# Kernel tuning notes

Hardware: AMD Instinct MI355X
Metric: run time of the kernel (lower is better)

## Reference

```python
import jax, jax.numpy as jnp
import numpy as np

B, S, H, NH = 2, 2048, 1024, 16
HD = H // NH  # 64


def setup_inputs() -> dict:
    key = jax.random.key(0)
    ks = jax.random.split(key, 9)
    s = 1.0 / np.sqrt(H)
    d = {"x": jax.random.normal(ks[0], (B, S, H), jnp.float32)}
    for i, n in enumerate(["Wq", "Wk", "Wv", "Wo"]):
        d[n] = jax.random.normal(ks[1 + i], (H, H), jnp.float32) * s
    for i, n in enumerate(["bq", "bk", "bv", "bo"]):
        d[n] = jax.random.normal(ks[5 + i], (H,), jnp.float32) * s
    return d


def _heads(x, W, b):
    # torch nn.Linear: y = x @ W.T + b, then split heads -> (B, NH, S, HD)
    y = x @ W.T + b
    return y.reshape(B, S, NH, HD).transpose(0, 2, 1, 3)


def _tetra_channels(t):
    # tetrapoint vector [a, 1-a, a*(1-a), clamp(1-(a+(1-a)),0,1)] for a scalar slice t
    a = jax.nn.sigmoid(t)
    na = 1.0 - a
    neither = jnp.clip(1.0 - (a + na), 0.0, 1.0)
    return jnp.stack([a, na, a * na, neither], axis=-1)  # (..., 4)


def reference(x, Wq, bq, Wk, bk, Wv, bv, Wo, bo):
    Q = _heads(x, Wq, bq)  # (B, NH, S, HD)
    K = _heads(x, Wk, bk)
    V = _heads(x, Wv, bv)
    # Original indexes Q_tetrapoints[:, :, :, 0] on [B,NH,S,HD,4]: selects head-dim
    # slot 0 (resp. 2) and keeps the 4 tetrapoint channels -> (B, NH, S, 4).
    Qa = _tetra_channels(Q[..., 0])
    Ka = _tetra_channels(K[..., 0])
    Qb = _tetra_channels(Q[..., 2])
    Kb = _tetra_channels(K[..., 2])
    scores = (jnp.einsum('bhsc,bhtc->bhst', Qa, Ka) / np.sqrt(HD)
              + 0.1 * jnp.einsum('bhsc,bhtc->bhst', Qb, Kb))  # (B, NH, S, S)
    w = jax.nn.softmax(scores, axis=-1)
    out = jnp.einsum('bhst,bhtd->bhsd', w, V)  # (B, NH, S, HD)
    out = out.transpose(0, 2, 1, 3).reshape(B, S, H)
    return out @ Wo.T + bo
```

## Files before the change

kernel.cpp:

```cpp
#include <hip/hip_runtime.h>
#include <hip/hip_bf16.h>

#define SS 2048
#define HH 1024
#define NHH 16
#define HDD 64

using f32x4  = __attribute__((ext_vector_type(4))) float;
using bf16x8 = __attribute__((ext_vector_type(8))) short;

#if __has_builtin(__builtin_amdgcn_exp2f)
#define EXP2F __builtin_amdgcn_exp2f
#else
#define EXP2F exp2f
#endif

__device__ __forceinline__ unsigned short f2bf(float f) {
    unsigned u = __builtin_bit_cast(unsigned, f);
    unsigned r = u + 0x7FFFu + ((u >> 16) & 1u);
    return (unsigned short)(r >> 16);
}

__device__ __forceinline__ unsigned bfround(float f) {
    unsigned u = __builtin_bit_cast(unsigned, f);
    return u + 0x7FFFu + ((u >> 16) & 1u);
}
__device__ __forceinline__ unsigned pack2bf(float a, float b) {
    return __builtin_amdgcn_perm(bfround(b), bfround(a), 0x07060302u);
}
__device__ __forceinline__ unsigned pack2bf_trunc(float a, float b) {
    return __builtin_amdgcn_perm(__builtin_bit_cast(unsigned, b),
                                 __builtin_bit_cast(unsigned, a), 0x07060302u);
}

__device__ __forceinline__ void tetra(float t, float* c) {
    float a = 1.f / (1.f + __expf(-t));
    float na = 1.f - a;
    float nei = 1.f - (a + na);
    nei = fminf(fmaxf(nei, 0.f), 1.f);
    c[0] = a; c[1] = na; c[2] = a * na; c[3] = nei;
}

__global__ __launch_bounds__(256) void cvt_kernel(
    const float* __restrict__ x, const float* __restrict__ Wv, const float* __restrict__ Wo,
    const float* __restrict__ Wq, const float* __restrict__ Wk,
    const float* __restrict__ bq, const float* __restrict__ bk,
    unsigned short* __restrict__ xb, unsigned short* __restrict__ Wvb, unsigned short* __restrict__ Wob,
    unsigned short* __restrict__ wselb, float* __restrict__ bselws)
{
    if (blockIdx.x >= 2048) {
        int n = blockIdx.x - 2048;
        int h = n >> 2, q = n & 3;
        int rowIdx = h * HDD + ((q & 1) ? 2 : 0);
        const float* src  = (q & 2) ? Wk : Wq;
        const float* bsrc = (q & 2) ? bk : bq;
        int t = threadIdx.x;
        float4 v = *(const float4*)(src + (size_t)rowIdx * HH + t * 4);
        uint2 pk;
        pk.x = pack2bf(v.x, v.y);
        pk.y = pack2bf(v.z, v.w);
        *(uint2*)(wselb + (size_t)n * HH + t * 4) = pk;
        if (t == 0) bselws[n] = bsrc[rowIdx];
        return;
    }
    size_t gid = (size_t)blockIdx.x * 256 + threadIdx.x;
    size_t base = gid * 8;
    {
        float4 a = *(const float4*)(x + base);
        float4 b = *(const float4*)(x + base + 4);
        uint4 pk;
        pk.x = pack2bf(a.x, a.y);
        pk.y = pack2bf(a.z, a.w);
        pk.z = pack2bf(b.x, b.y);
        pk.w = pack2bf(b.z, b.w);
        *(uint4*)(xb + base) = pk;
    }
    if (base < 1048576) {
        float4 a = *(const float4*)(Wv + base);
        float4 b = *(const float4*)(Wv + base + 4);
        uint4 pk;
        pk.x = pack2bf(a.x, a.y);
        pk.y = pack2bf(a.z, a.w);
        pk.z = pack2bf(b.x, b.y);
        pk.w = pack2bf(b.z, b.w);
        *(uint4*)(Wvb + base) = pk;
        a = *(const float4*)(Wo + base);
        b = *(const float4*)(Wo + base + 4);
        pk.x = pack2bf(a.x, a.y);
        pk.y = pack2bf(a.z, a.w);
        pk.z = pack2bf(b.x, b.y);
        pk.w = pack2bf(b.z, b.w);
        *(uint4*)(Wob + base) = pk;
    }
}

template<int OUT_MODE>
__device__ __forceinline__ void gemm_body(unsigned char* smem,
    const unsigned short* __restrict__ A, const unsigned short* __restrict__ Bw,
    const float* __restrict__ bias, void* __restrict__ Cout, int bx, int by)
{
    auto As = (unsigned short (*)[72])smem;
    auto Bs = (unsigned short (*)[72])(smem + 18432);
    int tid = threadIdx.x;
    int wave = tid >> 6, lane = tid & 63;
    int l15 = lane & 15, l16 = lane >> 4;
    int wm = wave >> 1, wn = wave & 1;
    int m0 = by * 128, n0 = bx * 64;

    int ar = tid >> 1, aseg = (tid & 1) * 32;
    int br = tid >> 2, bseg = (tid & 3) * 16;
    const unsigned short* Ap = A + (size_t)(m0 + ar) * HH + aseg;
    const unsigned short* Bp = Bw + (size_t)(n0 + br) * HH + bseg;

    f32x4 acc[4][2] = {};

    uint4 a0 = *(const uint4*)(Ap);
    uint4 a1 = *(const uint4*)(Ap + 8);
    uint4 a2 = *(const uint4*)(Ap + 16);
    uint4 a3 = *(const uint4*)(Ap + 24);
    uint4 b0 = *(const uint4*)(Bp);
    uint4 b1 = *(const uint4*)(Bp + 8);

    for (int k0 = 0; k0 < HH; k0 += 64) {
        __syncthreads();
        *(uint4*)&As[ar][aseg]      = a0;
        *(uint4*)&As[ar][aseg + 8]  = a1;
        *(uint4*)&As[ar][aseg + 16] = a2;
        *(uint4*)&As[ar][aseg + 24] = a3;
        *(uint4*)&Bs[br][bseg]      = b0;
        *(uint4*)&Bs[br][bseg + 8]  = b1;
        __syncthreads();

        int kn = (k0 + 64) & (HH - 1);
        uint4 na0 = *(const uint4*)(Ap + kn);
        uint4 na1 = *(const uint4*)(Ap + kn + 8);
        uint4 na2 = *(const uint4*)(Ap + kn + 16);
        uint4 na3 = *(const uint4*)(Ap + kn + 24);
        uint4 nb0 = *(const uint4*)(Bp + kn);
        uint4 nb1 = *(const uint4*)(Bp + kn + 8);

        #pragma unroll
        for (int kk = 0; kk < 64; kk += 32) {
            bf16x8 af[4], bfr[2];
            #pragma unroll
            for (int mi = 0; mi < 4; mi++)
                af[mi] = *(const bf16x8*)&As[wm * 64 + mi * 16 + l15][kk + l16 * 8];
            #pragma unroll
            for (int ni = 0; ni < 2; ni++)
                bfr[ni] = *(const bf16x8*)&Bs[wn * 32 + ni * 16 + l15][kk + l16 * 8];
            #pragma unroll
            for (int mi = 0; mi < 4; mi++)
                #pragma unroll
                for (int ni = 0; ni < 2; ni++)
                    acc[mi][ni] = __builtin_amdgcn_mfma_f32_16x16x32_bf16(af[mi], bfr[ni], acc[mi][ni], 0, 0, 0);
        }
        a0 = na0; a1 = na1; a2 = na2; a3 = na3; b0 = nb0; b1 = nb1;
    }

    float bv[2];
    #pragma unroll
    for (int ni = 0; ni < 2; ni++)
        bv[ni] = bias[n0 + wn * 32 + ni * 16 + l15];

    #pragma unroll
    for (int mi = 0; mi < 4; mi++) {
        #pragma unroll
        for (int ni = 0; ni < 2; ni++) {
            int n = n0 + wn * 32 + ni * 16 + l15;
            if (OUT_MODE == 0) {
                #pragma unroll
                for (int r = 0; r < 4; r++) {
                    int m = m0 + wm * 64 + mi * 16 + l16 * 4 + r;
                    ((float*)Cout)[(size_t)m * HH + n] = acc[mi][ni][r] + bv[ni];
                }
            } else {
                int m = m0 + wm * 64 + mi * 16 + l16 * 4;
                int b = m >> 11, s = m & 2047;
                int h = n >> 6, d = n & 63;
                uint2 pk;
                pk.x = pack2bf(acc[mi][ni][0] + bv[ni], acc[mi][ni][1] + bv[ni]);
                pk.y = pack2bf(acc[mi][ni][2] + bv[ni], acc[mi][ni][3] + bv[ni]);
                *(uint2*)((unsigned short*)Cout + ((size_t)((b * NHH + h) * HDD + d)) * SS + s) = pk;
            }
        }
    }
}

__device__ __forceinline__ void qk_body(unsigned char* smem,
    const unsigned short* __restrict__ xb, const unsigned short* __restrict__ wselb,
    const float* __restrict__ bselws,
    unsigned short* __restrict__ qfb, unsigned short* __restrict__ kfb, int blk)
{
    auto xs = (unsigned short (*)[72])smem;
    auto ws = (unsigned short (*)[72])(smem + 4608);
    auto ys = (float (*)[68])(smem + 13824);
    int tid = threadIdx.x;
    int wave = tid >> 6, lane = tid & 63;
    int l15 = lane & 15, l16 = lane >> 4;
    int m0 = blk * 32;
    int n0w = wave * 16;

    int xr = tid >> 3, xseg = (tid & 7) * 8;
    int wr = tid >> 2, wseg = (tid & 3) * 16;
    const unsigned short* xp = xb + (size_t)(m0 + xr) * HH + xseg;
    const unsigned short* wp = wselb + (size_t)wr * HH + wseg;

    f32x4 acc[2] = {};

    uint4 xv  = *(const uint4*)(xp);
    uint4 wv0 = *(const uint4*)(wp);
    uint4 wv1 = *(const uint4*)(wp + 8);

    for (int k0 = 0; k0 < HH; k0 += 64) {
        __syncthreads();
        *(uint4*)&xs[xr][xseg] = xv;
        *(uint4*)&ws[wr][wseg]     = wv0;
        *(uint4*)&ws[wr][wseg + 8] = wv1;
        __syncthreads();

        int kn = (k0 + 64) & (HH - 1);
        uint4 nxv  = *(const uint4*)(xp + kn);
        uint4 nwv0 = *(const uint4*)(wp + kn);
        uint4 nwv1 = *(const uint4*)(wp + kn + 8);

        #pragma unroll
        for (int kk = 0; kk < 64; kk += 32) {
            bf16x8 bfr = *(const bf16x8*)&ws[n0w + l15][kk + l16 * 8];
            #pragma unroll
            for (int mi = 0; mi < 2; mi++) {
                bf16x8 af = *(const bf16x8*)&xs[mi * 16 + l15][kk + l16 * 8];
                acc[mi] = __builtin_amdgcn_mfma_f32_16x16x32_bf16(af, bfr, acc[mi], 0, 0, 0);
            }
        }
        xv = nxv; wv0 = nwv0; wv1 = nwv1;
    }

    float bias = bselws[n0w + l15];
    __syncthreads();
    #pragma unroll
    for (int mi = 0; mi < 2; mi++)
        #pragma unroll
        for (int r = 0; r < 4; r++)
            ys[mi * 16 + l16 * 4 + r][n0w + l15] = acc[mi][r] + bias;
    __syncthreads();

    #pragma unroll
    for (int pass = 0; pass < 2; pass++) {
        int ml = tid & 31;
        int h = (tid >> 5) + pass * 8;
        float4 y4 = *(const float4*)&ys[ml][h * 4];
        float qa[4], qb2[4], ka[4], kb2[4];
        tetra(y4.x, qa);
        tetra(y4.y, qb2);
        tetra(y4.z, ka);
        tetra(y4.w, kb2);
        int m = m0 + ml, b = m >> 11, s = m & 2047;
        size_t base = ((size_t)(b * NHH + h) * SS + s) * 8;
        const float sA = 0.18033688011112042f;
        const float sB = 0.14426950408889634f;
        uint4 qp, kp;
        qp.x = pack2bf(qa[0] * sA, qa[1] * sA);
        qp.y = pack2bf(qa[2] * sA, qa[3] * sA);
        qp.z = pack2bf(qb2[0] * sB, qb2[1] * sB);
        qp.w = pack2bf(qb2[2] * sB, qb2[3] * sB);
        kp.x = pack2bf(ka[0], ka[1]);
        kp.y = pack2bf(ka[2], ka[3]);
        kp.z = pack2bf(kb2[0], kb2[1]);
        kp.w = pack2bf(kb2[2], kb2[3]);
        *(uint4*)(qfb + base) = qp;
        *(uint4*)(kfb + base) = kp;
    }
}

__global__ __launch_bounds__(256) void fused_mid(
    const unsigned short* __restrict__ xb,
    const unsigned short* __restrict__ Wvb, const float* __restrict__ bv,
    unsigned short* __restrict__ Vt,
    const unsigned short* __restrict__ wselb, const float* __restrict__ bselws,
    unsigned short* __restrict__ qfb, unsigned short* __restrict__ kfb)
{
    __shared__ __align__(16) unsigned char smem[27648];
    int id = blockIdx.x;
    if (id < 512)
        gemm_body<2>(smem, xb, Wvb, bv, Vt, id & 15, id >> 4);
    else
        qk_body(smem, xb, wselb, bselws, qfb, kfb, id - 512);
}

__global__ __launch_bounds__(256) void gemm_out(
    const unsigned short* __restrict__ A, const unsigned short* __restrict__ Bw,
    const float* __restrict__ bias, float* __restrict__ Cout)
{
    __shared__ __align__(16) unsigned char smem[27648];
    gemm_body<0>(smem, A, Bw, bias, Cout, blockIdx.x, blockIdx.y);
}

__global__ __launch_bounds__(256) void attn_mfma(
    const unsigned short* __restrict__ qfb, const unsigned short* __restrict__ kfb,
    const unsigned short* __restrict__ Vt, unsigned short* __restrict__ attnb)
{
    __shared__ unsigned short vt[2][64][72];
    __shared__ unsigned short ps[4][16][72];

    int tid = threadIdx.x;
    int wave = tid >> 6, lane = tid & 63;
    int l15 = lane & 15, l16 = lane >> 4;
    int bh = blockIdx.y, b = bh >> 4, h = bh & 15;
    int s0 = blockIdx.x * 64 + wave * 16;

    bf16x8 bfq = {0,0,0,0,0,0,0,0};
    if (l16 == 0)
        bfq = *(const bf16x8*)(qfb + ((size_t)bh * SS + s0 + l15) * 8);

    const short oneb = 0x3F80;
    bf16x8 ones = {oneb,oneb,oneb,oneb,oneb,oneb,oneb,oneb};

    const unsigned short* kfA = kfb + ((size_t)bh * SS + l15) * 8;
    int vd = tid >> 2, vseg = (tid & 3) * 16;
    const unsigned short* vsrc = Vt + ((size_t)bh * HDD + vd) * SS + vseg;

    f32x4 acc[4] = {};
    f32x4 accl = {};

    {
        uint4 t0a = *(const uint4*)(vsrc);
        uint4 t0b = *(const uint4*)(vsrc + 8);
        *(uint4*)&vt[0][vd][vseg]     = t0a;
        *(uint4*)&vt[0][vd][vseg + 8] = t0b;
    }
    uint4 sv0 = *(const uint4*)(vsrc + 64);
    uint4 sv1 = *(const uint4*)(vsrc + 64 + 8);
    bf16x8 kfr[4];
    #pragma unroll
    for (int tb = 0; tb < 4; tb++)
        kfr[tb] = *(const bf16x8*)(kfA + (size_t)(tb * 16) * 8);

    for (int it = 0; it < 32; it++) {
        int t0 = it << 6;
        __syncthreads();

        int nb = (it + 1) & 1;
        *(uint4*)&vt[nb][vd][vseg]     = sv0;
        *(uint4*)&vt[nb][vd][vseg + 8] = sv1;

        int tv = (t0 + 128) & (SS - 1);
        uint4 nv0 = *(const uint4*)(vsrc + tv);
        uint4 nv1 = *(const uint4*)(vsrc + tv + 8);
        int tkf = (t0 + 64) & (SS - 1);
        bf16x8 nkf[4];
        #pragma unroll
        for (int tb = 0; tb < 4; tb++)
            nkf[tb] = *(const bf16x8*)(kfA + (size_t)(tkf + tb * 16) * 8);

        #pragma unroll
        for (int tb = 0; tb < 4; tb++) {
            f32x4 sc = {};
            sc = __builtin_amdgcn_mfma_f32_16x16x32_bf16(kfr[tb], bfq, sc, 0, 0, 0);
            float p0 = EXP2F(sc[0]);
            float p1 = EXP2F(sc[1]);
            float p2 = EXP2F(sc[2]);
            float p3 = EXP2F(sc[3]);
            uint2 pw;
            pw.x = pack2bf_trunc(p0, p1);
            pw.y = pack2bf_trunc(p2, p3);
            *(uint2*)&ps[wave][l15][tb * 16 + l16 * 4] = pw;
        }

        int cb = it & 1;
        #pragma unroll
        for (int tk = 0; tk < 2; tk++) {
            bf16x8 ap = *(const bf16x8*)&ps[wave][l15][tk * 32 + l16 * 8];
            accl = __builtin_amdgcn_mfma_f32_16x16x32_bf16(ap, ones, accl, 0, 0, 0);
            #pragma unroll
            for (int nd = 0; nd < 4; nd++) {
                bf16x8 bv = *(const bf16x8*)&vt[cb][nd * 16 + l15][tk * 32 + l16 * 8];
                acc[nd] = __builtin_amdgcn_mfma_f32_16x16x32_bf16(ap, bv, acc[nd], 0, 0, 0);
            }
        }

        sv0 = nv0; sv1 = nv1;
        #pragma unroll
        for (int tb = 0; tb < 4; tb++) kfr[tb] = nkf[tb];
    }

    #pragma unroll
    for (int r = 0; r < 4; r++) {
        float linv = 1.f / accl[r];
        int q = s0 + l16 * 4 + r;
        size_t row = (size_t)(b * SS + q) * HH + h * HDD;
        #pragma unroll
        for (int nd = 0; nd < 4; nd++)
            attnb[row + nd * 16 + l15] = f2bf(acc[nd][r] * linv);
    }
}

extern "C" void kernel_launch(void* const* d_in, const int* in_sizes, int n_in,
                              void* d_out, int out_size, void* d_ws, size_t ws_size,
                              hipStream_t stream)
{
    const float* x  = (const float*)d_in[0];
    const float* Wq = (const float*)d_in[1];
    const float* Wk = (const float*)d_in[2];
    const float* Wv = (const float*)d_in[3];
    const float* Wo = (const float*)d_in[4];
    const float* bq = (const float*)d_in[5];
    const float* bk = (const float*)d_in[6];
    const float* bv = (const float*)d_in[7];
    const float* bo = (const float*)d_in[8];

    unsigned short* qfb   = (unsigned short*)d_ws;
    unsigned short* kfb   = qfb + 524288;
    unsigned short* xb    = kfb + 524288;
    unsigned short* attnb = xb;
    unsigned short* Wvb   = xb + 4194304;
    unsigned short* Wob   = Wvb + 1048576;
    unsigned short* Vt    = Wob + 1048576;
    unsigned short* wselb  = Vt + 4194304;
    float*          bselws = (float*)(wselb + 65536);

    cvt_kernel<<<2112, 256, 0, stream>>>(x, Wv, Wo, Wq, Wk, bq, bk, xb, Wvb, Wob, wselb, bselws);
    fused_mid<<<640, 256, 0, stream>>>(xb, Wvb, bv, Vt, wselb, bselws, qfb, kfb);
    attn_mfma<<<dim3(32, 32), 256, 0, stream>>>(qfb, kfb, Vt, attnb);
    gemm_out<<<dim3(16, 32), 256, 0, stream>>>(attnb, Wob, bo, (float*)d_out);
}
```

Measured before the change: 174.7 us.

## Process two query tiles per wave in attention, swizzle LDS, remap blocks

Each wave now handles 32 query rows instead of 16, so every V fragment loaded from LDS feeds two MFMAs and the grid halves to 512 blocks. The shared-memory layout for V and the probability tiles uses an XOR swizzle instead of padding, to avoid bank conflicts. Block indices are remapped so that blocks sharing a (batch, head) are spread across the interleaved block order, and s_setprio raises wave priority around the MFMA section. The cost is more accumulator registers and fewer blocks, which may lower occupancy.

```diff
diff --git a/kernel.cpp b/kernel.cpp
--- a/kernel.cpp
+++ b/kernel.cpp
@@ -299,34 +299,45 @@
     const unsigned short* __restrict__ qfb, const unsigned short* __restrict__ kfb,
     const unsigned short* __restrict__ Vt, unsigned short* __restrict__ attnb)
 {
-    __shared__ unsigned short vt[2][64][72];
-    __shared__ unsigned short ps[4][16][72];
+    __shared__ __align__(16) unsigned char lds[32768];
 
     int tid = threadIdx.x;
     int wave = tid >> 6, lane = tid & 63;
     int l15 = lane & 15, l16 = lane >> 4;
-    int bh = blockIdx.y, b = bh >> 4, h = bh & 15;
-    int s0 = blockIdx.x * 64 + wave * 16;
-
-    bf16x8 bfq = {0,0,0,0,0,0,0,0};
-    if (l16 == 0)
-        bfq = *(const bf16x8*)(qfb + ((size_t)bh * SS + s0 + l15) * 8);
+    int l7 = l15 & 7;
+
+    int L = blockIdx.x + (blockIdx.y << 4);
+    int logical = ((L & 7) << 6) + (L >> 3);
+    int bh = logical >> 4, qblk = logical & 15;
+    int b = bh >> 4, h = bh & 15;
+    int s0 = qblk * 128 + wave * 32;
+
+    bf16x8 qA = {0,0,0,0,0,0,0,0}, qB = {0,0,0,0,0,0,0,0};
+    if (l16 == 0) {
+        qA = *(const bf16x8*)(qfb + ((size_t)bh * SS + s0 + l15) * 8);
+        qB = *(const bf16x8*)(qfb + ((size_t)bh * SS + s0 + 16 + l15) * 8);
+    }
 
     const short oneb = 0x3F80;
     bf16x8 ones = {oneb,oneb,oneb,oneb,oneb,oneb,oneb,oneb};
 
     const unsigned short* kfA = kfb + ((size_t)bh * SS + l15) * 8;
-    int vd = tid >> 2, vseg = (tid & 3) * 16;
-    const unsigned short* vsrc = Vt + ((size_t)bh * HDD + vd) * SS + vseg;
-
-    f32x4 acc[4] = {};
-    f32x4 accl = {};
+    int vd = tid >> 2, vr = tid & 3;
+    const unsigned short* vsrc = Vt + ((size_t)bh * HDD + vd) * SS + vr * 16;
+
+    unsigned char* vrow = lds + vd * 128;
+    int sw0 = ((vr * 2)     ^ (vd & 7)) << 4;
+    int sw1 = ((vr * 2 + 1) ^ (vd & 7)) << 4;
+    unsigned char* psw = lds + 16384 + wave * 4096;
+
+    f32x4 acc[2][4] = {};
+    f32x4 accl[2] = {};
 
     {
         uint4 t0a = *(const uint4*)(vsrc);
         uint4 t0b = *(const uint4*)(vsrc + 8);
-        *(uint4*)&vt[0][vd][vseg]     = t0a;
-        *(uint4*)&vt[0][vd][vseg + 8] = t0b;
+        *(uint4*)(vrow + sw0) = t0a;
+        *(uint4*)(vrow + sw1) = t0b;
     }
     uint4 sv0 = *(const uint4*)(vsrc + 64);
     uint4 sv1 = *(const uint4*)(vsrc + 64 + 8);
@@ -340,8 +351,8 @@
         __syncthreads();
 
         int nb = (it + 1) & 1;
-        *(uint4*)&vt[nb][vd][vseg]     = sv0;
-        *(uint4*)&vt[nb][vd][vseg + 8] = sv1;
+        *(uint4*)(vrow + nb * 8192 + sw0) = sv0;
+        *(uint4*)(vrow + nb * 8192 + sw1) = sv1;
 
         int tv = (t0 + 128) & (SS - 1);
         uint4 nv0 = *(const uint4*)(vsrc + tv);
@@ -353,30 +364,39 @@
             nkf[tb] = *(const bf16x8*)(kfA + (size_t)(tkf + tb * 16) * 8);
 
         #pragma unroll
-        for (int tb = 0; tb < 4; tb++) {
-            f32x4 sc = {};
-            sc = __builtin_amdgcn_mfma_f32_16x16x32_bf16(kfr[tb], bfq, sc, 0, 0, 0);
-            float p0 = EXP2F(sc[0]);
-            float p1 = EXP2F(sc[1]);
-            float p2 = EXP2F(sc[2]);
-            float p3 = EXP2F(sc[3]);
-            uint2 pw;
-            pw.x = pack2bf_trunc(p0, p1);
-            pw.y = pack2bf_trunc(p2, p3);
-            *(uint2*)&ps[wave][l15][tb * 16 + l16 * 4] = pw;
+        for (int g = 0; g < 2; g++) {
+            bf16x8 qf = g ? qB : qA;
+            #pragma unroll
+            for (int tb = 0; tb < 4; tb++) {
+                f32x4 sc = {};
+                sc = __builtin_amdgcn_mfma_f32_16x16x32_bf16(kfr[tb], qf, sc, 0, 0, 0);
+                uint2 pw;
+                pw.x = pack2bf_trunc(EXP2F(sc[0]), EXP2F(sc[1]));
+                pw.y = pack2bf_trunc(EXP2F(sc[2]), EXP2F(sc[3]));
+                int qr = g * 16 + l15;
+                int c  = (tb * 2 + (l16 >> 1)) ^ l7;
+                *(uint2*)(psw + qr * 128 + c * 16 + (l16 & 1) * 8) = pw;
+            }
         }
 
         int cb = it & 1;
+        unsigned char* vbuf = lds + cb * 8192;
+        __builtin_amdgcn_s_setprio(1);
         #pragma unroll
         for (int tk = 0; tk < 2; tk++) {
-            bf16x8 ap = *(const bf16x8*)&ps[wave][l15][tk * 32 + l16 * 8];
-            accl = __builtin_amdgcn_mfma_f32_16x16x32_bf16(ap, ones, accl, 0, 0, 0);
+            int csw = ((tk * 4 + l16) ^ l7) << 4;
+            bf16x8 apA = *(const bf16x8*)(psw + l15 * 128 + csw);
+            bf16x8 apB = *(const bf16x8*)(psw + (16 + l15) * 128 + csw);
+            accl[0] = __builtin_amdgcn_mfma_f32_16x16x32_bf16(apA, ones, accl[0], 0, 0, 0);
+            accl[1] = __builtin_amdgcn_mfma_f32_16x16x32_bf16(apB, ones, accl[1], 0, 0, 0);
             #pragma unroll
             for (int nd = 0; nd < 4; nd++) {
-                bf16x8 bv = *(const bf16x8*)&vt[cb][nd * 16 + l15][tk * 32 + l16 * 8];
-                acc[nd] = __builtin_amdgcn_mfma_f32_16x16x32_bf16(ap, bv, acc[nd], 0, 0, 0);
+                bf16x8 bv = *(const bf16x8*)(vbuf + (nd * 16 + l15) * 128 + csw);
+                acc[0][nd] = __builtin_amdgcn_mfma_f32_16x16x32_bf16(apA, bv, acc[0][nd], 0, 0, 0);
+                acc[1][nd] = __builtin_amdgcn_mfma_f32_16x16x32_bf16(apB, bv, acc[1][nd], 0, 0, 0);
             }
         }
+        __builtin_amdgcn_s_setprio(0);
 
         sv0 = nv0; sv1 = nv1;
         #pragma unroll
@@ -384,13 +404,16 @@
     }
 
     #pragma unroll
-    for (int r = 0; r < 4; r++) {
-        float linv = 1.f / accl[r];
-        int q = s0 + l16 * 4 + r;
-        size_t row = (size_t)(b * SS + q) * HH + h * HDD;
-        #pragma unroll
-        for (int nd = 0; nd < 4; nd++)
-            attnb[row + nd * 16 + l15] = f2bf(acc[nd][r] * linv);
+    for (int g = 0; g < 2; g++) {
+        #pragma unroll
+        for (int r = 0; r < 4; r++) {
+            float linv = 1.f / accl[g][r];
+            int q = s0 + g * 16 + l16 * 4 + r;
+            size_t row = (size_t)(b * SS + q) * HH + h * HDD;
+            #pragma unroll
+            for (int nd = 0; nd < 4; nd++)
+                attnb[row + nd * 16 + l15] = f2bf(acc[g][nd][r] * linv);
+        }
     }
 }
 
@@ -420,6 +443,6 @@
 
     cvt_kernel<<<2112, 256, 0, stream>>>(x, Wv, Wo, Wq, Wk, bq, bk, xb, Wvb, Wob, wselb, bselws);
     fused_mid<<<640, 256, 0, stream>>>(xb, Wvb, bv, Vt, wselb, bselws, qfb, kfb);
-    attn_mfma<<<dim3(32, 32), 256, 0, stream>>>(qfb, kfb, Vt, attnb);
+    attn_mfma<<<dim3(16, 32), 256, 0, stream>>>(qfb, kfb, Vt, attnb);
     gemm_out<<<dim3(16, 32), 256, 0, stream>>>(attnb, Wob, bo, (float*)d_out);
 }
```

After: 169.0 us. 3.2% less time.
